# Performance work log

Hardware: AMD Instinct MI355X
Metric: run time of the kernel (lower is better)

The kernel has to match this reference:

```python
import jax, jax.numpy as jnp
import numpy as np

D = 1024       # embedding_dim
H = 16         # num_attention_heads
B = 2
S = 2048       # seq_len == context_len


def setup_inputs() -> dict:
    key = jax.random.key(0)
    k1, k2, k3 = jax.random.split(key, 3)
    X = jax.random.normal(k1, (B, S, D), dtype=jnp.float32)
    W_qkv = jax.random.normal(k2, (D, 3 * D), dtype=jnp.float32) * 0.02
    b_qkv = jnp.zeros((3 * D,), dtype=jnp.float32)
    W_out = jax.random.normal(k3, (D, D), dtype=jnp.float32) * 0.02
    b_out = jnp.zeros((D,), dtype=jnp.float32)
    return {"X": X, "W_qkv": W_qkv, "b_qkv": b_qkv, "W_out": W_out, "b_out": b_out}


def reference(X, W_qkv, b_qkv, W_out, b_out):
    b, s, d = X.shape
    hd = d // H
    # fused QKV projection (GPT-2 Conv1D == x @ W + b)
    qkv = X @ W_qkv + b_qkv                       # [b, s, 3d]
    q, k, v = jnp.split(qkv, 3, axis=2)
    # [b, h, s, hd]
    q = q.reshape(b, s, H, hd).transpose(0, 2, 1, 3)
    k = k.reshape(b, s, H, hd).transpose(0, 2, 1, 3)
    v = v.reshape(b, s, H, hd).transpose(0, 2, 1, 3)
    # NOTE: source scales by rsqrt(embedding_dim), not head_dim
    scale = 1.0 / jnp.sqrt(jnp.float32(d))
    scores = jnp.einsum("bhqd,bhkd->bhqk", q, k) * scale
    causal = jnp.tril(jnp.ones((s, s), dtype=bool))
    scores = jnp.where(causal[None, None], scores, -jnp.inf)
    # attention_dropout applied pre-softmax in source; identity at eval (p used here = 0)
    probs = jax.nn.softmax(scores, axis=-1)
    attn = jnp.einsum("bhqk,bhkd->bhqd", probs, v)
    attn = attn.transpose(0, 2, 1, 3).reshape(b, s, d)
    out = attn @ W_out + b_out                    # outwards proj; dropout eval = identity
    return out
```

## Files before the change

### kernel.cpp

```cpp
#include <hip/hip_runtime.h>

#define S_LEN 2048
#define DIM   1024
#define NHEAD 16
#define HDIM  64

typedef __attribute__((ext_vector_type(8))) short  short8;
typedef __attribute__((ext_vector_type(4))) float  floatx4;
typedef __attribute__((ext_vector_type(4))) unsigned short ushort4v;

#define Q_PRESCALE 0.045084220027780106f

__device__ inline unsigned short f2bf(float f) {
  unsigned v = __builtin_bit_cast(unsigned, f);
  v += 0x7FFFu + ((v >> 16) & 1u);
  return (unsigned short)(v >> 16);
}

__device__ inline void async16(const unsigned short* g, unsigned short* l) {
  __builtin_amdgcn_global_load_lds(
      (const __attribute__((address_space(1))) unsigned int*)g,
      (__attribute__((address_space(3))) unsigned int*)l, 16, 0, 0);
}

__global__ __launch_bounds__(256) void cvt_kernel(
    const float* __restrict__ in, unsigned short* __restrict__ out, int n) {
  int i = (blockIdx.x * 256 + threadIdx.x) * 8;
  if (i >= n) return;
  float4 a = *(const float4*)&in[i];
  float4 b = *(const float4*)&in[i + 4];
  short8 o;
  o[0] = (short)f2bf(a.x); o[1] = (short)f2bf(a.y);
  o[2] = (short)f2bf(a.z); o[3] = (short)f2bf(a.w);
  o[4] = (short)f2bf(b.x); o[5] = (short)f2bf(b.y);
  o[6] = (short)f2bf(b.z); o[7] = (short)f2bf(b.w);
  *(short8*)&out[i] = o;
}

__global__ __launch_bounds__(256) void cvtT_kernel(
    const float* __restrict__ in, unsigned short* __restrict__ out, int K, int N) {
  __shared__ unsigned short tile[32][33];
  int n0 = blockIdx.x * 32, k0 = blockIdx.y * 32;
  int tx = threadIdx.x, ty = threadIdx.y;
#pragma unroll
  for (int i = 0; i < 32; i += 8)
    tile[ty + i][tx] = f2bf(in[(size_t)(k0 + ty + i) * N + n0 + tx]);
  __syncthreads();
#pragma unroll
  for (int i = 0; i < 32; i += 8)
    out[(size_t)(n0 + ty + i) * K + k0 + tx] = tile[tx][ty + i];
}

#define GEMM128_BODY(APTR, BPTR)                                                   \
  __shared__ __align__(16) unsigned short As[128][64];                             \
  __shared__ __align__(16) unsigned short Bs[128][64];                             \
  const int m0 = blockIdx.y * 128, n0 = blockIdx.x * 128;                          \
  const int t = threadIdx.x, lane = t & 63, wave = t >> 6;                         \
  const int quad = lane >> 4, l16 = lane & 15;                                     \
  const int wm = (wave >> 1) * 64, wn = (wave & 1) * 64;                           \
  const int lr = lane >> 3, lc = lane & 7, sc8 = (lc ^ lr) * 8;                    \
  const int sw = l16 & 7;                                                          \
  const int pA0 = (quad ^ sw) * 8, pA1 = ((4 + quad) ^ sw) * 8;                    \
  floatx4 acc[4][4];                                                               \
  _Pragma("unroll") for (int mi = 0; mi < 4; mi++)                                 \
      _Pragma("unroll") for (int ni = 0; ni < 4; ni++)                             \
          acc[mi][ni] = (floatx4){0.f, 0.f, 0.f, 0.f};                             \
  for (int k0 = 0; k0 < DIM; k0 += 64) {                                           \
    _Pragma("unroll") for (int i = 0; i < 4; i++) {                                \
      int rb = wave * 32 + i * 8;                                                  \
      async16(&APTR[(size_t)(m0 + rb + lr) * DIM + k0 + sc8], &As[rb][0]);         \
      async16(&BPTR[(size_t)(n0 + rb + lr) * DIM + k0 + sc8], &Bs[rb][0]);         \
    }                                                                              \
    __syncthreads();                                                               \
    short8 a0[4], a1[4];                                                           \
    _Pragma("unroll") for (int mi = 0; mi < 4; mi++) {                             \
      int row = wm + mi * 16 + l16;                                                \
      a0[mi] = *(const short8*)&As[row][pA0];                                      \
      a1[mi] = *(const short8*)&As[row][pA1];                                      \
    }                                                                              \
    _Pragma("unroll") for (int ni = 0; ni < 4; ni++) {                             \
      int row = wn + ni * 16 + l16;                                                \
      short8 b0 = *(const short8*)&Bs[row][pA0];                                   \
      short8 b1 = *(const short8*)&Bs[row][pA1];                                   \
      _Pragma("unroll") for (int mi = 0; mi < 4; mi++) {                           \
        acc[mi][ni] = __builtin_amdgcn_mfma_f32_16x16x32_bf16(a0[mi], b0, acc[mi][ni], 0, 0, 0); \
        acc[mi][ni] = __builtin_amdgcn_mfma_f32_16x16x32_bf16(a1[mi], b1, acc[mi][ni], 0, 0, 0); \
      }                                                                            \
    }                                                                              \
    __syncthreads();                                                               \
  }

__global__ __launch_bounds__(256) void gemm_qkv128(
    const unsigned short* __restrict__ Xb,
    const unsigned short* __restrict__ Wt,
    const float* __restrict__ bias,
    unsigned short* __restrict__ Qg,
    unsigned short* __restrict__ Kg,
    unsigned short* __restrict__ Vgt) {
  GEMM128_BODY(Xb, Wt)
  const int section = n0 >> 10;
  const int head = ((n0 + wn) >> 6) & 15;
#pragma unroll
  for (int mi = 0; mi < 4; mi++) {
    int mg = m0 + wm + mi * 16 + quad * 4;
    int bb = mg >> 11, sb = mg & 2047;
    size_t y = (size_t)bb * NHEAD + head;
    if (section == 2) {
#pragma unroll
      for (int ni = 0; ni < 4; ni++) {
        int hdi = ni * 16 + l16;
        float bv = bias[n0 + wn + hdi];
        ushort4v o;
#pragma unroll
        for (int r = 0; r < 4; r++) o[r] = f2bf(acc[mi][ni][r] + bv);
        *(ushort4v*)&Vgt[(y * HDIM + hdi) * S_LEN + sb] = o;
      }
    } else if (section == 0) {
#pragma unroll
      for (int ni = 0; ni < 4; ni++) {
        int hdi = ni * 16 + l16;
        float bv = bias[n0 + wn + hdi];
#pragma unroll
        for (int r = 0; r < 4; r++)
          Qg[(y * S_LEN + sb + r) * HDIM + hdi] = f2bf((acc[mi][ni][r] + bv) * Q_PRESCALE);
      }
    } else {
#pragma unroll
      for (int ni = 0; ni < 4; ni++) {
        int hdi = ni * 16 + l16;
        float bv = bias[n0 + wn + hdi];
#pragma unroll
        for (int r = 0; r < 4; r++)
          Kg[(y * S_LEN + sb + r) * HDIM + hdi] = f2bf(acc[mi][ni][r] + bv);
      }
    }
  }
}

__global__ __launch_bounds__(256) void gemm_out128(
    const unsigned short* __restrict__ A,
    const unsigned short* __restrict__ Wt,
    const float* __restrict__ bias,
    float* __restrict__ outp) {
  GEMM128_BODY(A, Wt)
#pragma unroll
  for (int ni = 0; ni < 4; ni++) {
    int n = n0 + wn + ni * 16 + l16;
    float bv = bias[n];
#pragma unroll
    for (int mi = 0; mi < 4; mi++) {
      int mg = m0 + wm + mi * 16 + quad * 4;
#pragma unroll
      for (int r = 0; r < 4; r++)
        outp[(size_t)(mg + r) * DIM + n] = acc[mi][ni][r] + bv;
    }
  }
}

__global__ __launch_bounds__(256) void gemm_qkv_kernel(
    const float* __restrict__ X,
    const unsigned short* __restrict__ Wt,
    const float* __restrict__ bias,
    unsigned short* __restrict__ Qg,
    unsigned short* __restrict__ Kg,
    unsigned short* __restrict__ Vgt,
    int g0, int G) {
  __shared__ __align__(16) unsigned short As[64][72];
  __shared__ __align__(16) unsigned short Bs[64][72];
  const int tn = blockIdx.x;
  const int section = tn / G, within = tn % G;
  const int n0 = section * 1024 + (g0 + within) * 64;
  const int m0 = blockIdx.y * 64;
  const int t = threadIdx.x, lane = t & 63, wave = t >> 6;
  const int quad = lane >> 4, l16 = lane & 15;

  floatx4 acc[4];
#pragma unroll
  for (int i = 0; i < 4; i++) acc[i] = (floatx4){0.f, 0.f, 0.f, 0.f};

  for (int k0 = 0; k0 < DIM; k0 += 64) {
#pragma unroll
    for (int i = 0; i < 2; i++) {
      int v = t + i * 256;
      int row = v >> 3, cc = (v & 7) * 8;
      float4 f0 = *(const float4*)&X[(size_t)(m0 + row) * DIM + k0 + cc];
      float4 f1 = *(const float4*)&X[(size_t)(m0 + row) * DIM + k0 + cc + 4];
      short8 o;
      o[0] = (short)f2bf(f0.x); o[1] = (short)f2bf(f0.y);
      o[2] = (short)f2bf(f0.z); o[3] = (short)f2bf(f0.w);
      o[4] = (short)f2bf(f1.x); o[5] = (short)f2bf(f1.y);
      o[6] = (short)f2bf(f1.z); o[7] = (short)f2bf(f1.w);
      *(short8*)&As[row][cc] = o;
      *(short8*)&Bs[row][cc] = *(const short8*)&Wt[(size_t)(n0 + row) * DIM + k0 + cc];
    }
    __syncthreads();
    short8 a0 = *(const short8*)&As[wave * 16 + l16][quad * 8];
    short8 a1 = *(const short8*)&As[wave * 16 + l16][32 + quad * 8];
#pragma unroll
    for (int nt = 0; nt < 4; nt++) {
      short8 b0 = *(const short8*)&Bs[nt * 16 + l16][quad * 8];
      short8 b1 = *(const short8*)&Bs[nt * 16 + l16][32 + quad * 8];
      acc[nt] = __builtin_amdgcn_mfma_f32_16x16x32_bf16(a0, b0, acc[nt], 0, 0, 0);
      acc[nt] = __builtin_amdgcn_mfma_f32_16x16x32_bf16(a1, b1, acc[nt], 0, 0, 0);
    }
    __syncthreads();
  }

  const int mbase = m0 + wave * 16 + quad * 4;
  const int b = mbase >> 11, sbase = mbase & 2047;
  const int y = b * G + within;
  if (section == 2) {
#pragma unroll
    for (int nt = 0; nt < 4; nt++) {
      int hdi = nt * 16 + l16;
      float bv = bias[n0 + hdi];
      ushort4v o;
#pragma unroll
      for (int r = 0; r < 4; r++) o[r] = f2bf(acc[nt][r] + bv);
      *(ushort4v*)&Vgt[((size_t)y * HDIM + hdi) * S_LEN + sbase] = o;
    }
  } else if (section == 0) {
#pragma unroll
    for (int nt = 0; nt < 4; nt++) {
      int hdi = nt * 16 + l16;
      float bv = bias[n0 + hdi];
#pragma unroll
      for (int r = 0; r < 4; r++)
        Qg[((size_t)y * S_LEN + sbase + r) * HDIM + hdi] =
            f2bf((acc[nt][r] + bv) * Q_PRESCALE);
    }
  } else {
#pragma unroll
    for (int nt = 0; nt < 4; nt++) {
      int hdi = nt * 16 + l16;
      float bv = bias[n0 + hdi];
#pragma unroll
      for (int r = 0; r < 4; r++)
        Kg[((size_t)y * S_LEN + sbase + r) * HDIM + hdi] = f2bf(acc[nt][r] + bv);
    }
  }
}

__global__ __launch_bounds__(256) void attn_kernel(
    const unsigned short* __restrict__ Qg,
    const unsigned short* __restrict__ Kg,
    const unsigned short* __restrict__ Vgt,
    unsigned short* __restrict__ attnB) {
  __shared__ __align__(16) unsigned short Ks[2][64][64];
  __shared__ __align__(16) unsigned short Vs[2][64][64];
  __shared__ __align__(16) unsigned short Ones[16][64];
  __shared__ __align__(16) unsigned short Ps[4][16][72];

  const int y = blockIdx.x;
  const int b = y >> 4, h = y & 15;
  const int qt = 31 - blockIdx.y;
  const int q0 = qt * 64;
  const int nT = qt + 1;
  const int t = threadIdx.x;
  const int lane = t & 63, wave = t >> 6;
  const int quad = lane >> 4, l16 = lane & 15;
  const int lr = lane >> 3, lc = lane & 7;
  const int sc8 = (lc ^ lr) * 8;
  const int sw = l16 & 7;
  const int p0 = (quad ^ sw) * 8, p1 = ((4 + quad) ^ sw) * 8;

  const unsigned short* Qh = Qg + (size_t)y * S_LEN * HDIM;
  const unsigned short* Kh = Kg + (size_t)y * S_LEN * HDIM;
  const unsigned short* Vh = Vgt + (size_t)y * HDIM * S_LEN;

  if (t < 128) {
    int row = t >> 3, c = (t & 7) * 8;
    unsigned short vv = (row == 0) ? (unsigned short)0x3F80 : (unsigned short)0;
    short8 o;
#pragma unroll
    for (int j = 0; j < 8; j++) o[j] = (short)vv;
    *(short8*)&Ones[row][c] = o;
  }

  short8 aq0, aq1;
  {
    const unsigned short* qp = &Qh[(size_t)(q0 + wave * 16 + l16) * HDIM];
    aq0 = *(const short8*)&qp[quad * 8];
    aq1 = *(const short8*)&qp[32 + quad * 8];
  }

  floatx4 o_acc[5];
#pragma unroll
  for (int dt = 0; dt < 5; dt++) o_acc[dt] = (floatx4){0.f, 0.f, 0.f, 0.f};

  {
    int rb = wave * 16;
#pragma unroll
    for (int i = 0; i < 2; i++) {
      async16(&Kh[(size_t)(rb + i * 8 + lr) * HDIM + sc8], &Ks[0][rb + i * 8][0]);
      async16(&Vh[(size_t)(rb + i * 8 + lr) * S_LEN + sc8], &Vs[0][rb + i * 8][0]);
    }
  }

  for (int tt = 0; tt < nT; tt++) {
    const int j0 = tt * 64;
    const int buf = tt & 1;
    __syncthreads();
    if (tt + 1 < nT) {
      int j1 = j0 + 64, nb = 1 - buf;
      int rb = wave * 16;
#pragma unroll
      for (int i = 0; i < 2; i++) {
        async16(&Kh[(size_t)(j1 + rb + i * 8 + lr) * HDIM + sc8], &Ks[nb][rb + i * 8][0]);
        async16(&Vh[(size_t)(rb + i * 8 + lr) * S_LEN + j1 + sc8], &Vs[nb][rb + i * 8][0]);
      }
    }

    floatx4 sc[4];
#pragma unroll
    for (int nt = 0; nt < 4; nt++) {
      short8 kb0 = *(const short8*)&Ks[buf][nt * 16 + l16][p0];
      short8 kb1 = *(const short8*)&Ks[buf][nt * 16 + l16][p1];
      sc[nt] = (floatx4){0.f, 0.f, 0.f, 0.f};
      sc[nt] = __builtin_amdgcn_mfma_f32_16x16x32_bf16(aq0, kb0, sc[nt], 0, 0, 0);
      sc[nt] = __builtin_amdgcn_mfma_f32_16x16x32_bf16(aq1, kb1, sc[nt], 0, 0, 0);
    }

    if (j0 == q0) {
#pragma unroll
      for (int nt = 0; nt < 4; nt++) {
        int keyl = nt * 16 + l16;
#pragma unroll
        for (int r = 0; r < 4; r++) {
          int ql = wave * 16 + quad * 4 + r;
          float p = exp2f(sc[nt][r]);
          p = (keyl <= ql) ? p : 0.f;
          Ps[wave][quad * 4 + r][nt * 16 + l16] = f2bf(p);
        }
      }
    } else {
#pragma unroll
      for (int nt = 0; nt < 4; nt++)
#pragma unroll
        for (int r = 0; r < 4; r++)
          Ps[wave][quad * 4 + r][nt * 16 + l16] = f2bf(exp2f(sc[nt][r]));
    }
    short8 ap0 = *(const short8*)&Ps[wave][l16][quad * 8];
    short8 ap1 = *(const short8*)&Ps[wave][l16][32 + quad * 8];

#pragma unroll
    for (int dt = 0; dt < 5; dt++) {
      short8 vb0 = (dt < 4) ? *(const short8*)&Vs[buf][dt * 16 + l16][p0]
                            : *(const short8*)&Ones[l16][p0];
      short8 vb1 = (dt < 4) ? *(const short8*)&Vs[buf][dt * 16 + l16][p1]
                            : *(const short8*)&Ones[l16][p1];
      o_acc[dt] = __builtin_amdgcn_mfma_f32_16x16x32_bf16(ap0, vb0, o_acc[dt], 0, 0, 0);
      o_acc[dt] = __builtin_amdgcn_mfma_f32_16x16x32_bf16(ap1, vb1, o_acc[dt], 0, 0, 0);
    }
  }

  float linv[4];
#pragma unroll
  for (int r = 0; r < 4; r++)
    linv[r] = 1.0f / __shfl(o_acc[4][r], quad << 4);
#pragma unroll
  for (int dt = 0; dt < 4; dt++) {
#pragma unroll
    for (int r = 0; r < 4; r++) {
      int qg = q0 + wave * 16 + quad * 4 + r;
      attnB[(size_t)(b * S_LEN + qg) * DIM + h * HDIM + dt * 16 + l16] =
          f2bf(o_acc[dt][r] * linv[r]);
    }
  }
}

extern "C" void kernel_launch(void* const* d_in, const int* in_sizes, int n_in,
                              void* d_out, int out_size, void* d_ws, size_t ws_size,
                              hipStream_t stream) {
  const float* X    = (const float*)d_in[0];
  const float* Wqkv = (const float*)d_in[1];
  const float* bqkv = (const float*)d_in[2];
  const float* Wout = (const float*)d_in[3];
  const float* bout = (const float*)d_in[4];
  float* outp = (float*)d_out;

  unsigned short* Wqkvt = (unsigned short*)d_ws;
  unsigned short* Woutt = Wqkvt + (size_t)3145728;
  unsigned short* attnB = Woutt + (size_t)1048576;
  unsigned short* Qg    = attnB + (size_t)4194304;
  unsigned short* Kg    = Qg + (size_t)4194304;
  unsigned short* Vgt   = Kg + (size_t)4194304;
  unsigned short* Xb    = Vgt + (size_t)4194304;

  const bool bigWs = ws_size >= (size_t)48 * 1024 * 1024;

  cvtT_kernel<<<dim3(3072 / 32, 1024 / 32), dim3(32, 8), 0, stream>>>(Wqkv, Wqkvt, 1024, 3072);
  cvtT_kernel<<<dim3(1024 / 32, 1024 / 32), dim3(32, 8), 0, stream>>>(Wout, Woutt, 1024, 1024);

  if (bigWs) {
    cvt_kernel<<<4194304 / (256 * 8), 256, 0, stream>>>(X, Xb, 4194304);
    gemm_qkv128<<<dim3(3072 / 128, 4096 / 128), 256, 0, stream>>>(
        Xb, Wqkvt, bqkv, Qg, Kg, Vgt);
  } else {
    gemm_qkv_kernel<<<dim3(48, 64), 256, 0, stream>>>(
        X, Wqkvt, bqkv, Qg, Kg, Vgt, 0, 16);
  }
  attn_kernel<<<dim3(32, 32), 256, 0, stream>>>(Qg, Kg, Vgt, attnB);
  gemm_out128<<<dim3(1024 / 128, 4096 / 128), 256, 0, stream>>>(attnB, Woutt, bout, outp);
}
```

Baseline: 193.8 us.

## Fuse whole attention pipeline into one cooperative persistent kernel with grid syncs

Replaces the six separate launches (weight/X conversion, QKV GEMM, attention, output GEMM) with one cooperative kernel of 256 blocks × 512 threads that runs every stage and separates them with grid.sync. The attention stage pairs a short and a long causal query block per workgroup to balance work, and the GEMMs use 512-thread tiles. This removes launch gaps and tail effects between stages, but adds grid-barrier cost and forces fewer, larger blocks, which may lower per-stage efficiency and occupancy. It falls back to the separate kernels if the cooperative launch fails.

```diff
diff --git a/kernel.cpp b/kernel.cpp
--- a/kernel.cpp
+++ b/kernel.cpp
@@ -1,15 +1,17 @@
 #include <hip/hip_runtime.h>
+#include <hip/hip_cooperative_groups.h>
+
+namespace cg = cooperative_groups;
 
 #define S_LEN 2048
 #define DIM   1024
 #define NHEAD 16
 #define HDIM  64
+#define Q_PRESCALE 0.045084220027780106f
 
 typedef __attribute__((ext_vector_type(8))) short  short8;
 typedef __attribute__((ext_vector_type(4))) float  floatx4;
 typedef __attribute__((ext_vector_type(4))) unsigned short ushort4v;
-
-#define Q_PRESCALE 0.045084220027780106f
 
 __device__ inline unsigned short f2bf(float f) {
   unsigned v = __builtin_bit_cast(unsigned, f);
@@ -21,6 +23,301 @@
   __builtin_amdgcn_global_load_lds(
       (const __attribute__((address_space(1))) unsigned int*)g,
       (__attribute__((address_space(3))) unsigned int*)l, 16, 0, 0);
+}
+
+__global__ __launch_bounds__(512, 2) void fused_kernel(
+    const float* __restrict__ X, const float* __restrict__ Wqkv,
+    const float* __restrict__ bqkv, const float* __restrict__ Wout,
+    const float* __restrict__ bout, float* __restrict__ outp,
+    unsigned short* __restrict__ Wqkvt, unsigned short* __restrict__ Woutt,
+    unsigned short* __restrict__ attnB, unsigned short* __restrict__ Qg,
+    unsigned short* __restrict__ Kg, unsigned short* __restrict__ Vgt,
+    unsigned short* __restrict__ Xb) {
+  cg::grid_group grid = cg::this_grid();
+  __shared__ __align__(16) unsigned char smem[53248];
+  const int T = threadIdx.x;
+  const int bId = blockIdx.x;
+  const int lane = T & 63, wave = T >> 6;
+  const int quad = lane >> 4, l16 = lane & 15;
+  const int lr = lane >> 3, lc = lane & 7;
+  const int sc8v = (lc ^ lr) * 8;
+  const int sw = l16 & 7;
+  const int p0 = (quad ^ sw) * 8, p1 = ((4 + quad) ^ sw) * 8;
+
+  {
+    for (size_t i = ((size_t)bId * 512 + T) * 8; i < (size_t)4194304;
+         i += (size_t)256 * 512 * 8) {
+      float4 a = *(const float4*)&X[i];
+      float4 b = *(const float4*)&X[i + 4];
+      short8 o;
+      o[0] = (short)f2bf(a.x); o[1] = (short)f2bf(a.y);
+      o[2] = (short)f2bf(a.z); o[3] = (short)f2bf(a.w);
+      o[4] = (short)f2bf(b.x); o[5] = (short)f2bf(b.y);
+      o[6] = (short)f2bf(b.z); o[7] = (short)f2bf(b.w);
+      *(short8*)&Xb[i] = o;
+    }
+    const int sub = T >> 8, tid = T & 255;
+    unsigned short (*tile)[33] = (unsigned short (*)[33])(smem + sub * 2112);
+    const int tx = tid & 31, ty = tid >> 5;
+    for (int ti = bId * 2 + sub; ti < 4096; ti += 512) {
+      const float* in; unsigned short* out; int N, tn, tk;
+      if (ti < 3072) { in = Wqkv; out = Wqkvt; N = 3072; tn = ti % 96; tk = ti / 96; }
+      else { int u = ti - 3072; in = Wout; out = Woutt; N = 1024; tn = u & 31; tk = u >> 5; }
+      int n0 = tn * 32, k0 = tk * 32;
+#pragma unroll
+      for (int i = 0; i < 32; i += 8)
+        tile[ty + i][tx] = f2bf(in[(size_t)(k0 + ty + i) * N + n0 + tx]);
+      __syncthreads();
+#pragma unroll
+      for (int i = 0; i < 32; i += 8)
+        out[(size_t)(n0 + ty + i) * 1024 + k0 + tx] = tile[tx][ty + i];
+      __syncthreads();
+    }
+  }
+  __threadfence();
+  grid.sync();
+
+  {
+    unsigned short (*As)[64] = (unsigned short (*)[64])smem;
+    unsigned short (*Bs)[64] = (unsigned short (*)[64])(smem + 16384);
+    const int wm = (wave & 3) * 32, wn = (wave >> 2) * 64;
+    for (int j = 0; j < 3; j++) {
+      const int ti = bId * 3 + j;
+      const int m0 = (ti / 24) * 128, n0 = (ti % 24) * 128;
+      floatx4 acc[2][4];
+#pragma unroll
+      for (int mi = 0; mi < 2; mi++)
+#pragma unroll
+        for (int ni = 0; ni < 4; ni++) acc[mi][ni] = (floatx4){0.f, 0.f, 0.f, 0.f};
+      for (int k0 = 0; k0 < DIM; k0 += 64) {
+        const int rb = wave * 16;
+        async16(&Xb[(size_t)(m0 + rb + lr) * DIM + k0 + sc8v], &As[rb][0]);
+        async16(&Xb[(size_t)(m0 + rb + 8 + lr) * DIM + k0 + sc8v], &As[rb + 8][0]);
+        async16(&Wqkvt[(size_t)(n0 + rb + lr) * DIM + k0 + sc8v], &Bs[rb][0]);
+        async16(&Wqkvt[(size_t)(n0 + rb + 8 + lr) * DIM + k0 + sc8v], &Bs[rb + 8][0]);
+        __syncthreads();
+        short8 a0[2], a1[2];
+#pragma unroll
+        for (int mi = 0; mi < 2; mi++) {
+          int row = wm + mi * 16 + l16;
+          a0[mi] = *(const short8*)&As[row][p0];
+          a1[mi] = *(const short8*)&As[row][p1];
+        }
+#pragma unroll
+        for (int ni = 0; ni < 4; ni++) {
+          int row = wn + ni * 16 + l16;
+          short8 b0 = *(const short8*)&Bs[row][p0];
+          short8 b1 = *(const short8*)&Bs[row][p1];
+#pragma unroll
+          for (int mi = 0; mi < 2; mi++) {
+            acc[mi][ni] = __builtin_amdgcn_mfma_f32_16x16x32_bf16(a0[mi], b0, acc[mi][ni], 0, 0, 0);
+            acc[mi][ni] = __builtin_amdgcn_mfma_f32_16x16x32_bf16(a1[mi], b1, acc[mi][ni], 0, 0, 0);
+          }
+        }
+        __syncthreads();
+      }
+      const int section = n0 >> 10;
+      const int head = ((n0 + wn) >> 6) & 15;
+#pragma unroll
+      for (int mi = 0; mi < 2; mi++) {
+        int mg = m0 + wm + mi * 16 + quad * 4;
+        int bb = mg >> 11, sb = mg & 2047;
+        size_t y = (size_t)bb * NHEAD + head;
+        if (section == 2) {
+#pragma unroll
+          for (int ni = 0; ni < 4; ni++) {
+            int hdi = ni * 16 + l16;
+            float bv = bqkv[n0 + wn + hdi];
+            ushort4v o;
+#pragma unroll
+            for (int r = 0; r < 4; r++) o[r] = f2bf(acc[mi][ni][r] + bv);
+            *(ushort4v*)&Vgt[(y * HDIM + hdi) * S_LEN + sb] = o;
+          }
+        } else if (section == 0) {
+#pragma unroll
+          for (int ni = 0; ni < 4; ni++) {
+            int hdi = ni * 16 + l16;
+            float bv = bqkv[n0 + wn + hdi];
+#pragma unroll
+            for (int r = 0; r < 4; r++)
+              Qg[(y * S_LEN + sb + r) * HDIM + hdi] = f2bf((acc[mi][ni][r] + bv) * Q_PRESCALE);
+          }
+        } else {
+#pragma unroll
+          for (int ni = 0; ni < 4; ni++) {
+            int hdi = ni * 16 + l16;
+            float bv = bqkv[n0 + wn + hdi];
+#pragma unroll
+            for (int r = 0; r < 4; r++)
+              Kg[(y * S_LEN + sb + r) * HDIM + hdi] = f2bf(acc[mi][ni][r] + bv);
+          }
+        }
+      }
+    }
+  }
+  __threadfence();
+  grid.sync();
+
+  {
+    unsigned short (*Ks)[64][64] = (unsigned short (*)[64][64])smem;
+    unsigned short (*Vs)[64][64] = (unsigned short (*)[64][64])(smem + 16384);
+    unsigned short (*Ones)[64]   = (unsigned short (*)[64])(smem + 32768);
+    unsigned short (*Ps)[16][72] = (unsigned short (*)[16][72])(smem + 34816);
+    const int y = bId >> 3, ii = bId & 7;
+    const int b = y >> 4, h = y & 15;
+    const unsigned short* Qh = Qg + (size_t)y * S_LEN * HDIM;
+    const unsigned short* Kh = Kg + (size_t)y * S_LEN * HDIM;
+    const unsigned short* Vh = Vgt + (size_t)y * HDIM * S_LEN;
+
+    if (T < 128) {
+      int row = T >> 3, c = (T & 7) * 8;
+      unsigned short vv = (row == 0) ? (unsigned short)0x3F80 : (unsigned short)0;
+      short8 o;
+#pragma unroll
+      for (int jj = 0; jj < 8; jj++) o[jj] = (short)vv;
+      *(short8*)&Ones[row][c] = o;
+    }
+
+    const int nT1 = 2 * ii + 2;
+    short8 aq0, aq1;
+    floatx4 o_acc[5];
+    {
+      const int rb = wave * 8;
+      async16(&Kh[(size_t)(rb + lr) * HDIM + sc8v], &Ks[0][rb][0]);
+      async16(&Vh[(size_t)(rb + lr) * S_LEN + sc8v], &Vs[0][rb][0]);
+    }
+    for (int s = 0; s < 34; s++) {
+      const bool first = (s < nT1);
+      const int qb = first ? ii : 15 - ii;
+      const int tt = first ? s : s - nT1;
+      const int q0 = qb * 128, j0 = tt * 64;
+      if (tt == 0) {
+        const unsigned short* qp = &Qh[(size_t)(q0 + wave * 16 + l16) * HDIM];
+        aq0 = *(const short8*)&qp[quad * 8];
+        aq1 = *(const short8*)&qp[32 + quad * 8];
+#pragma unroll
+        for (int dt = 0; dt < 5; dt++) o_acc[dt] = (floatx4){0.f, 0.f, 0.f, 0.f};
+      }
+      const int buf = s & 1;
+      __syncthreads();
+      if (s + 1 < 34) {
+        const int tt2 = (s + 1 < nT1) ? s + 1 : s + 1 - nT1;
+        const int j1 = tt2 * 64, nb = 1 - buf;
+        const int rb = wave * 8;
+        async16(&Kh[(size_t)(j1 + rb + lr) * HDIM + sc8v], &Ks[nb][rb][0]);
+        async16(&Vh[(size_t)(rb + lr) * S_LEN + j1 + sc8v], &Vs[nb][rb][0]);
+      }
+      const int W0 = q0 + wave * 16;
+      if (j0 <= W0 + 15) {
+        floatx4 sc[4];
+#pragma unroll
+        for (int nt = 0; nt < 4; nt++) {
+          short8 kb0 = *(const short8*)&Ks[buf][nt * 16 + l16][p0];
+          short8 kb1 = *(const short8*)&Ks[buf][nt * 16 + l16][p1];
+          sc[nt] = (floatx4){0.f, 0.f, 0.f, 0.f};
+          sc[nt] = __builtin_amdgcn_mfma_f32_16x16x32_bf16(aq0, kb0, sc[nt], 0, 0, 0);
+          sc[nt] = __builtin_amdgcn_mfma_f32_16x16x32_bf16(aq1, kb1, sc[nt], 0, 0, 0);
+        }
+        if (j0 + 63 <= W0) {
+#pragma unroll
+          for (int nt = 0; nt < 4; nt++)
+#pragma unroll
+            for (int r = 0; r < 4; r++)
+              Ps[wave][quad * 4 + r][nt * 16 + l16] = f2bf(exp2f(sc[nt][r]));
+        } else {
+#pragma unroll
+          for (int nt = 0; nt < 4; nt++) {
+            int keyg = j0 + nt * 16 + l16;
+#pragma unroll
+            for (int r = 0; r < 4; r++) {
+              int qg = W0 + quad * 4 + r;
+              float p = exp2f(sc[nt][r]);
+              p = (keyg <= qg) ? p : 0.f;
+              Ps[wave][quad * 4 + r][nt * 16 + l16] = f2bf(p);
+            }
+          }
+        }
+        short8 ap0 = *(const short8*)&Ps[wave][l16][quad * 8];
+        short8 ap1 = *(const short8*)&Ps[wave][l16][32 + quad * 8];
+#pragma unroll
+        for (int dt = 0; dt < 5; dt++) {
+          short8 vb0 = (dt < 4) ? *(const short8*)&Vs[buf][dt * 16 + l16][p0]
+                                : *(const short8*)&Ones[l16][p0];
+          short8 vb1 = (dt < 4) ? *(const short8*)&Vs[buf][dt * 16 + l16][p1]
+                                : *(const short8*)&Ones[l16][p1];
+          o_acc[dt] = __builtin_amdgcn_mfma_f32_16x16x32_bf16(ap0, vb0, o_acc[dt], 0, 0, 0);
+          o_acc[dt] = __builtin_amdgcn_mfma_f32_16x16x32_bf16(ap1, vb1, o_acc[dt], 0, 0, 0);
+        }
+      }
+      if (tt == 2 * qb + 1) {
+        float linv[4];
+#pragma unroll
+        for (int r = 0; r < 4; r++)
+          linv[r] = 1.0f / __shfl(o_acc[4][r], quad << 4);
+#pragma unroll
+        for (int dt = 0; dt < 4; dt++)
+#pragma unroll
+          for (int r = 0; r < 4; r++) {
+            int qg = q0 + wave * 16 + quad * 4 + r;
+            attnB[(size_t)(b * S_LEN + qg) * DIM + h * HDIM + dt * 16 + l16] =
+                f2bf(o_acc[dt][r] * linv[r]);
+          }
+      }
+    }
+  }
+  __threadfence();
+  grid.sync();
+
+  {
+    unsigned short (*As)[64] = (unsigned short (*)[64])smem;
+    unsigned short (*Bs)[64] = (unsigned short (*)[64])(smem + 16384);
+    const int wm = (wave & 3) * 32, wn = (wave >> 2) * 64;
+    const int m0 = (bId >> 3) * 128, n0 = (bId & 7) * 128;
+    floatx4 acc[2][4];
+#pragma unroll
+    for (int mi = 0; mi < 2; mi++)
+#pragma unroll
+      for (int ni = 0; ni < 4; ni++) acc[mi][ni] = (floatx4){0.f, 0.f, 0.f, 0.f};
+    for (int k0 = 0; k0 < DIM; k0 += 64) {
+      const int rb = wave * 16;
+      async16(&attnB[(size_t)(m0 + rb + lr) * DIM + k0 + sc8v], &As[rb][0]);
+      async16(&attnB[(size_t)(m0 + rb + 8 + lr) * DIM + k0 + sc8v], &As[rb + 8][0]);
+      async16(&Woutt[(size_t)(n0 + rb + lr) * DIM + k0 + sc8v], &Bs[rb][0]);
+      async16(&Woutt[(size_t)(n0 + rb + 8 + lr) * DIM + k0 + sc8v], &Bs[rb + 8][0]);
+      __syncthreads();
+      short8 a0[2], a1[2];
+#pragma unroll
+      for (int mi = 0; mi < 2; mi++) {
+        int row = wm + mi * 16 + l16;
+        a0[mi] = *(const short8*)&As[row][p0];
+        a1[mi] = *(const short8*)&As[row][p1];
+      }
+#pragma unroll
+      for (int ni = 0; ni < 4; ni++) {
+        int row = wn + ni * 16 + l16;
+        short8 b0 = *(const short8*)&Bs[row][p0];
+        short8 b1 = *(const short8*)&Bs[row][p1];
+#pragma unroll
+        for (int mi = 0; mi < 2; mi++) {
+          acc[mi][ni] = __builtin_amdgcn_mfma_f32_16x16x32_bf16(a0[mi], b0, acc[mi][ni], 0, 0, 0);
+          acc[mi][ni] = __builtin_amdgcn_mfma_f32_16x16x32_bf16(a1[mi], b1, acc[mi][ni], 0, 0, 0);
+        }
+      }
+      __syncthreads();
+    }
+#pragma unroll
+    for (int ni = 0; ni < 4; ni++) {
+      int n = n0 + wn + ni * 16 + l16;
+      float bv = bout[n];
+#pragma unroll
+      for (int mi = 0; mi < 2; mi++) {
+        int mg = m0 + wm + mi * 16 + quad * 4;
+#pragma unroll
+        for (int r = 0; r < 4; r++)
+          outp[(size_t)(mg + r) * DIM + n] = acc[mi][ni][r] + bv;
+      }
+    }
+  }
 }
 
 __global__ __launch_bounds__(256) void cvt_kernel(
@@ -157,90 +454,6 @@
   }
 }
 
-__global__ __launch_bounds__(256) void gemm_qkv_kernel(
-    const float* __restrict__ X,
-    const unsigned short* __restrict__ Wt,
-    const float* __restrict__ bias,
-    unsigned short* __restrict__ Qg,
-    unsigned short* __restrict__ Kg,
-    unsigned short* __restrict__ Vgt,
-    int g0, int G) {
-  __shared__ __align__(16) unsigned short As[64][72];
-  __shared__ __align__(16) unsigned short Bs[64][72];
-  const int tn = blockIdx.x;
-  const int section = tn / G, within = tn % G;
-  const int n0 = section * 1024 + (g0 + within) * 64;
-  const int m0 = blockIdx.y * 64;
-  const int t = threadIdx.x, lane = t & 63, wave = t >> 6;
-  const int quad = lane >> 4, l16 = lane & 15;
-
-  floatx4 acc[4];
-#pragma unroll
-  for (int i = 0; i < 4; i++) acc[i] = (floatx4){0.f, 0.f, 0.f, 0.f};
-
-  for (int k0 = 0; k0 < DIM; k0 += 64) {
-#pragma unroll
-    for (int i = 0; i < 2; i++) {
-      int v = t + i * 256;
-      int row = v >> 3, cc = (v & 7) * 8;
-      float4 f0 = *(const float4*)&X[(size_t)(m0 + row) * DIM + k0 + cc];
-      float4 f1 = *(const float4*)&X[(size_t)(m0 + row) * DIM + k0 + cc + 4];
-      short8 o;
-      o[0] = (short)f2bf(f0.x); o[1] = (short)f2bf(f0.y);
-      o[2] = (short)f2bf(f0.z); o[3] = (short)f2bf(f0.w);
-      o[4] = (short)f2bf(f1.x); o[5] = (short)f2bf(f1.y);
-      o[6] = (short)f2bf(f1.z); o[7] = (short)f2bf(f1.w);
-      *(short8*)&As[row][cc] = o;
-      *(short8*)&Bs[row][cc] = *(const short8*)&Wt[(size_t)(n0 + row) * DIM + k0 + cc];
-    }
-    __syncthreads();
-    short8 a0 = *(const short8*)&As[wave * 16 + l16][quad * 8];
-    short8 a1 = *(const short8*)&As[wave * 16 + l16][32 + quad * 8];
-#pragma unroll
-    for (int nt = 0; nt < 4; nt++) {
-      short8 b0 = *(const short8*)&Bs[nt * 16 + l16][quad * 8];
-      short8 b1 = *(const short8*)&Bs[nt * 16 + l16][32 + quad * 8];
-      acc[nt] = __builtin_amdgcn_mfma_f32_16x16x32_bf16(a0, b0, acc[nt], 0, 0, 0);
-      acc[nt] = __builtin_amdgcn_mfma_f32_16x16x32_bf16(a1, b1, acc[nt], 0, 0, 0);
-    }
-    __syncthreads();
-  }
-
-  const int mbase = m0 + wave * 16 + quad * 4;
-  const int b = mbase >> 11, sbase = mbase & 2047;
-  const int y = b * G + within;
-  if (section == 2) {
-#pragma unroll
-    for (int nt = 0; nt < 4; nt++) {
-      int hdi = nt * 16 + l16;
-      float bv = bias[n0 + hdi];
-      ushort4v o;
-#pragma unroll
-      for (int r = 0; r < 4; r++) o[r] = f2bf(acc[nt][r] + bv);
-      *(ushort4v*)&Vgt[((size_t)y * HDIM + hdi) * S_LEN + sbase] = o;
-    }
-  } else if (section == 0) {
-#pragma unroll
-    for (int nt = 0; nt < 4; nt++) {
-      int hdi = nt * 16 + l16;
-      float bv = bias[n0 + hdi];
-#pragma unroll
-      for (int r = 0; r < 4; r++)
-        Qg[((size_t)y * S_LEN + sbase + r) * HDIM + hdi] =
-            f2bf((acc[nt][r] + bv) * Q_PRESCALE);
-    }
-  } else {
-#pragma unroll
-    for (int nt = 0; nt < 4; nt++) {
-      int hdi = nt * 16 + l16;
-      float bv = bias[n0 + hdi];
-#pragma unroll
-      for (int r = 0; r < 4; r++)
-        Kg[((size_t)y * S_LEN + sbase + r) * HDIM + hdi] = f2bf(acc[nt][r] + bv);
-    }
-  }
-}
-
 __global__ __launch_bounds__(256) void attn_kernel(
     const unsigned short* __restrict__ Qg,
     const unsigned short* __restrict__ Kg,
@@ -359,14 +572,13 @@
   for (int r = 0; r < 4; r++)
     linv[r] = 1.0f / __shfl(o_acc[4][r], quad << 4);
 #pragma unroll
-  for (int dt = 0; dt < 4; dt++) {
+  for (int dt = 0; dt < 4; dt++)
 #pragma unroll
     for (int r = 0; r < 4; r++) {
       int qg = q0 + wave * 16 + quad * 4 + r;
       attnB[(size_t)(b * S_LEN + qg) * DIM + h * HDIM + dt * 16 + l16] =
           f2bf(o_acc[dt][r] * linv[r]);
     }
-  }
 }
 
 extern "C" void kernel_launch(void* const* d_in, const int* in_sizes, int n_in,
@@ -387,19 +599,18 @@
   unsigned short* Vgt   = Kg + (size_t)4194304;
   unsigned short* Xb    = Vgt + (size_t)4194304;
 
-  const bool bigWs = ws_size >= (size_t)48 * 1024 * 1024;
-
-  cvtT_kernel<<<dim3(3072 / 32, 1024 / 32), dim3(32, 8), 0, stream>>>(Wqkv, Wqkvt, 1024, 3072);
-  cvtT_kernel<<<dim3(1024 / 32, 1024 / 32), dim3(32, 8), 0, stream>>>(Wout, Woutt, 1024, 1024);
-
-  if (bigWs) {
-    cvt_kernel<<<4194304 / (256 * 8), 256, 0, stream>>>(X, Xb, 4194304);
-    gemm_qkv128<<<dim3(3072 / 128, 4096 / 128), 256, 0, stream>>>(
-        Xb, Wqkvt, bqkv, Qg, Kg, Vgt);
-  } else {
-    gemm_qkv_kernel<<<dim3(48, 64), 256, 0, stream>>>(
-        X, Wqkvt, bqkv, Qg, Kg, Vgt, 0, 16);
-  }
+  void* args[] = {(void*)&X, (void*)&Wqkv, (void*)&bqkv, (void*)&Wout, (void*)&bout,
+                  (void*)&outp, (void*)&Wqkvt, (void*)&Woutt, (void*)&attnB,
+                  (void*)&Qg, (void*)&Kg, (void*)&Vgt, (void*)&Xb};
+  hipError_t err = hipLaunchCooperativeKernel((const void*)fused_kernel,
+                                              dim3(256), dim3(512), args, 0, stream);
+  if (err == hipSuccess) return;
+  (void)hipGetLastError();
+
+  cvtT_kernel<<<dim3(96, 32), dim3(32, 8), 0, stream>>>(Wqkv, Wqkvt, 1024, 3072);
+  cvtT_kernel<<<dim3(32, 32), dim3(32, 8), 0, stream>>>(Wout, Woutt, 1024, 1024);
+  cvt_kernel<<<4194304 / (256 * 8), 256, 0, stream>>>(X, Xb, 4194304);
+  gemm_qkv128<<<dim3(24, 32), 256, 0, stream>>>(Xb, Wqkvt, bqkv, Qg, Kg, Vgt);
   attn_kernel<<<dim3(32, 32), 256, 0, stream>>>(Qg, Kg, Vgt, attnB);
-  gemm_out128<<<dim3(1024 / 128, 4096 / 128), 256, 0, stream>>>(attnB, Woutt, bout, outp);
-}
+  gemm_out128<<<dim3(8, 32), 256, 0, stream>>>(attnB, Woutt, bout, outp);
+}
```

Result: slower. 468.6 us (+141.8%).
